# Performance work log

Measured on AMD Instinct MI355X. Metric: run time of the kernel, lower is better.

Reference implementation:

```python
import jax, jax.numpy as jnp
import numpy as np

N = 100000
E = 1600000
IN_DIM = 1024
H_DIM = 16
DIM2 = H_DIM * 8  # 128


def _xavier(key, shape):
    fan_in, fan_out = shape[-2], shape[-1]
    lim = (6.0 / (fan_in + fan_out)) ** 0.5
    return jax.random.uniform(key, shape, jnp.float32, -lim, lim)


def setup_inputs() -> dict:
    key = jax.random.key(0)
    ks = jax.random.split(key, 10)
    x = jax.random.normal(ks[0], (N, IN_DIM), jnp.float32)
    edge_index = jax.random.randint(ks[1], (2, E), 0, N)
    perm = jax.random.permutation(ks[2], N)
    W1 = _xavier(ks[3], (IN_DIM, DIM2)); b1 = jnp.zeros((DIM2,), jnp.float32)
    W2 = _xavier(ks[4], (DIM2, DIM2)); b2 = jnp.zeros((DIM2,), jnp.float32)
    W3 = _xavier(ks[5], (DIM2, H_DIM)); b3 = jnp.zeros((H_DIM,), jnp.float32)
    Wdo = _xavier(ks[6], (1, DIM2, DIM2)); bdo = jnp.zeros((1,), jnp.float32)
    Wdh = _xavier(ks[7], (1, H_DIM, H_DIM)); bdh = jnp.zeros((1,), jnp.float32)
    return dict(x=x, W1=W1, b1=b1, W2=W2, b2=b2, W3=W3, b3=b3,
                Wdo=Wdo, bdo=bdo, Wdh=Wdh, bdh=bdh,
                edge_index=edge_index, perm=perm)


def _graph_conv(x, W, b, src, dst, norm_src, norm_dst):
    # DGL GraphConv, norm='both': D_dst^{-1/2} A D_src^{-1/2} X W + b
    h = (x * norm_src[:, None]) @ W          # mult W first (in >= out)
    agg = jax.ops.segment_sum(h[src], dst, num_segments=N)
    return agg * norm_dst[:, None] + b


def _l2norm(x):
    n = jnp.sqrt(jnp.sum(x * x, axis=1, keepdims=True))
    return x / jnp.maximum(n, 1e-12)


def _bilinear(a, c, W, b):
    # nn.Bilinear(n_h, n_h, 1): out[n,k] = a[n] @ W[k] @ c[n] + b[k]
    return jnp.einsum('nd,kde,ne->nk', a, W, c) + b


def reference(x, W1, b1, W2, b2, W3, b3, Wdo, bdo, Wdh, bdh, edge_index, perm):
    src, dst = edge_index[0], edge_index[1]
    ones = jnp.ones((E,), jnp.float32)
    deg_out = jnp.maximum(jax.ops.segment_sum(ones, src, num_segments=N), 1.0)
    deg_in = jnp.maximum(jax.ops.segment_sum(ones, dst, num_segments=N), 1.0)
    ns, nd = deg_out ** -0.5, deg_in ** -0.5

    def encode(xin):
        o = _graph_conv(xin, W1, b1, src, dst, ns, nd)
        o = _graph_conv(o, W2, b2, src, dst, ns, nd) + o
        h = _graph_conv(o, W3, b3, src, dst, ns, nd)
        emb_o = jax.nn.relu(o)
        g_o = jax.nn.sigmoid(_l2norm(emb_o))
        emb_h = jax.nn.relu(h)
        g_h = jax.nn.sigmoid(_l2norm(emb_h))
        return h, emb_o, g_o, emb_h, g_h

    h, emb_o, g_o, emb_h, g_h = encode(x)
    h_a, emb_oa, g_oa, emb_ha, g_ha = encode(x[perm])

    def disc(c, h_pl, h_mi, W, b):
        return jnp.concatenate([_bilinear(h_pl, c, W, b), _bilinear(h_mi, c, W, b)], axis=1)

    ret_o = disc(g_o, emb_o, emb_oa, Wdo, bdo)
    ret_oa = disc(g_oa, emb_oa, emb_o, Wdo, bdo)
    ret_h = disc(g_h, emb_h, emb_ha, Wdh, bdh)
    ret_ha = disc(g_ha, emb_ha, emb_h, Wdh, bdh)
    return (h, ret_o, ret_h, ret_oa, ret_ha)
```

## Files before the change

kernel.cpp:

```cpp
#include <hip/hip_runtime.h>
#include <math.h>

#define NN 100000
#define EE 1600000
#define SCB 98
#define GB1 782
#define FB 3125

typedef __attribute__((ext_vector_type(8))) short bf16x8;
typedef __attribute__((ext_vector_type(4))) short bf16x4;
typedef __attribute__((ext_vector_type(4))) float f32x4;

__device__ __forceinline__ unsigned short f2bf(float x){
  union { float f; unsigned u; } v; v.f = x;
  unsigned r = v.u + 0x7FFFu + ((v.u >> 16) & 1u);
  return (unsigned short)(r >> 16);
}
__device__ __forceinline__ float bf2f(unsigned short h){
  union { unsigned u; float f; } v; v.u = ((unsigned)h) << 16; return v.f;
}
__device__ __forceinline__ float sigm(float x){ return 1.0f/(1.0f+__expf(-x)); }

__device__ __forceinline__ void barrier_lds_only(){
  asm volatile("s_waitcnt lgkmcnt(0)" ::: "memory");
  __builtin_amdgcn_s_barrier();
  __builtin_amdgcn_sched_barrier(0);
}

__global__ __launch_bounds__(256) void k_deg_wcvt(const int* __restrict__ src, const int* __restrict__ dst,
                      int* __restrict__ dout, int* __restrict__ din,
                      const float* __restrict__ W1, const float* __restrict__ W2,
                      const float* __restrict__ Wdo, const float* __restrict__ W3,
                      unsigned short* __restrict__ W1T, unsigned short* __restrict__ W2T,
                      unsigned short* __restrict__ WdoB, unsigned short* __restrict__ W3c){
  int b = blockIdx.x;
  if (b < EE/256){
    int e = b*256 + threadIdx.x;
    atomicAdd(&dout[src[e]],1); atomicAdd(&din[dst[e]],1);
  } else {
    int i = (b - EE/256)*256 + threadIdx.x;
    if (i < 131072){
      int c = i>>13, r = i&8191, col = r>>6, k = c*64 + (r&63);
      W1T[i] = f2bf(W1[(size_t)k*128 + col]);
    } else if (i < 147456){
      int j = i-131072;
      int c = j>>13, r = j&8191, col = r>>6, k = c*64 + (r&63);
      W2T[j] = f2bf(W2[(size_t)k*128 + col]);
    } else if (i < 163840){
      int j = i-147456;
      int c = j>>13, r = j&8191, col = r>>6, k = c*64 + (r&63);
      WdoB[j] = f2bf(Wdo[(size_t)col*128 + k]);
    } else if (i < 165888){
      int j = i-163840;
      int col = j>>7, k = j&127;
      W3c[j] = f2bf(W3[(size_t)k*16 + col]);
    }
  }
}

__global__ __launch_bounds__(1024) void k_scan1(const int* __restrict__ din, int* __restrict__ chunk,
                        int* __restrict__ bsum){
  __shared__ int wsum[16];
  int t = threadIdx.x, lane = t & 63, w = t >> 6;
  int i = blockIdx.x*1024 + t;
  int v = (i < NN) ? din[i] : 0;
  int x = v;
  #pragma unroll
  for (int off=1; off<64; off<<=1){
    int y = __shfl_up(x, off);
    if (lane>=off) x += y;
  }
  if (lane==63) wsum[w] = x;
  __syncthreads();
  int pre = 0;
  #pragma unroll
  for (int j=0;j<16;j++) if (j<w) pre += wsum[j];
  int incl = x + pre;
  if (i < NN) chunk[i] = incl;
  if (t == 1023) bsum[blockIdx.x] = incl;
}

__global__ __launch_bounds__(128) void k_scan2(const int* __restrict__ bsum, int* __restrict__ bpre,
                       int* __restrict__ row_ptr){
  __shared__ int w0tot;
  int t = threadIdx.x, lane = t & 63, w = t >> 6;
  int v = (t < SCB) ? bsum[t] : 0;
  int x = v;
  #pragma unroll
  for (int off=1; off<64; off<<=1){
    int y = __shfl_up(x, off);
    if (lane>=off) x += y;
  }
  if (w==0 && lane==63) w0tot = x;
  __syncthreads();
  int incl = x + (w ? w0tot : 0);
  if (t < SCB) bpre[t] = incl - v;
  if (t == 0) row_ptr[0] = 0;
}

__global__ __launch_bounds__(256) void k_scan3(const int* __restrict__ din, const int* __restrict__ chunk,
                       const int* __restrict__ bpre, const int* __restrict__ dout,
                       const int* __restrict__ perm,
                       int* __restrict__ row_ptr, int* __restrict__ cursor,
                       float* __restrict__ ns, float* __restrict__ nd, int* __restrict__ inv){
  int i = blockIdx.x*256 + threadIdx.x;
  if (i < NN){
    int d = din[i];
    int val = chunk[i] + bpre[i>>10];
    row_ptr[i+1] = val;
    cursor[i] = val - d;
    ns[i] = rsqrtf((float)max(dout[i],1));
    nd[i] = rsqrtf((float)max(d,1));
    inv[perm[i]] = i;
  }
}

__global__ __launch_bounds__(512,4) void k_g1fill(
    const float* __restrict__ A, const unsigned short* __restrict__ Wc,
    unsigned short* __restrict__ tz,
    const int* __restrict__ src, const int* __restrict__ dst,
    int* __restrict__ cursor, int* __restrict__ col)
{
  constexpr int NC = 16;
  __shared__ __align__(16) unsigned short As[2*128*72];
  __shared__ __align__(16) unsigned short Bs[2*128*64];
  if (blockIdx.x >= GB1){
    int e = (blockIdx.x - GB1)*512 + threadIdx.x;
    if (e < EE){
      int pos = atomicAdd(&cursor[dst[e]],1);
      col[pos] = src[e];
    }
    return;
  }
  int t = threadIdx.x, wave = t>>6, lane = t&63;
  int row0 = blockIdx.x*128;

  int srow = t>>4;
  int scol4 = (t&15)*4;
  int colB = t>>2;
  int s0B = (t&3)*2;

  f32x4 acc[8] = {};
  float4 S0[4], S1[4];
  bf16x8 w0{}, w1{};

#define ALOAD(SET, CC) { \
  _Pragma("unroll") \
  for (int p=0;p<4;p++){ \
    int rr = min(row0 + p*32 + srow, NN-1); \
    SET[p] = *(const float4*)(A + (size_t)rr*1024 + (CC)*64 + scol4); } }

#define AWRITE(SET, BUF) { \
  _Pragma("unroll") \
  for (int p=0;p<4;p++){ \
    short4 s4; \
    s4.x = (short)f2bf(SET[p].x); s4.y = (short)f2bf(SET[p].y); \
    s4.z = (short)f2bf(SET[p].z); s4.w = (short)f2bf(SET[p].w); \
    *(short4*)&As[(BUF)*9216 + (p*32+srow)*72 + scol4] = s4; } }

#define BLOAD(CC) { \
  const unsigned short* gp = Wc + (size_t)(CC)*8192 + (size_t)t*16; \
  w0 = *(const bf16x8*)(gp); \
  w1 = *(const bf16x8*)(gp+8); }

#define BWRITE(BUF) { \
  unsigned short* bb = &Bs[(BUF)*8192]; \
  *(bf16x8*)&bb[colB*64 + ((s0B     ^ (colB&7))<<3)] = w0; \
  *(bf16x8*)&bb[colB*64 + (((s0B+1) ^ (colB&7))<<3)] = w1; }

  ALOAD(S0, 0);
  BLOAD(0);
  AWRITE(S0, 0);
  BWRITE(0);
  ALOAD(S1, 1);
  BLOAD(1);
  barrier_lds_only();

  int slot0 = lane>>4;
  int c = lane & 15;
  int arow = wave*16 + (lane&15);
  #pragma unroll
  for (int cc=0; cc<NC; ++cc){
    if (cc+2 < NC){
      if (cc&1) { ALOAD(S1, cc+2); } else { ALOAD(S0, cc+2); }
    }
    int cur = cc&1;
    const unsigned short* ab = &As[cur*9216];
    const unsigned short* bb = &Bs[cur*8192];
    {
      bf16x8 af = *(const bf16x8*)&ab[arow*72 + (slot0<<3)];
      #pragma unroll
      for (int j=0;j<8;j++){
        int cj = j*16 + c;
        bf16x8 b = *(const bf16x8*)&bb[cj*64 + ((slot0 ^ (cj&7))<<3)];
        acc[j] = __builtin_amdgcn_mfma_f32_16x16x32_bf16(af, b, acc[j], 0, 0, 0);
      }
    }
    {
      bf16x8 af = *(const bf16x8*)&ab[arow*72 + 32 + (slot0<<3)];
      #pragma unroll
      for (int j=0;j<8;j++){
        int cj = j*16 + c;
        bf16x8 b = *(const bf16x8*)&bb[cj*64 + (((slot0+4) ^ (cj&7))<<3)];
        acc[j] = __builtin_amdgcn_mfma_f32_16x16x32_bf16(af, b, acc[j], 0, 0, 0);
      }
    }
    if (cc+1 < NC){
      int nb = (cc+1)&1;
      if (cc&1) { AWRITE(S0, nb); } else { AWRITE(S1, nb); }
      BWRITE(nb);
      barrier_lds_only();
      if (cc+2 < NC) BLOAD(cc+2);
    }
  }
#undef ALOAD
#undef AWRITE
#undef BLOAD
#undef BWRITE

  int rbase = row0 + wave*16 + (lane>>4)*4;
  #pragma unroll
  for (int j=0;j<8;j++){
    int colx = j*16 + c;
    #pragma unroll
    for (int r=0;r<4;r++){
      int row = rbase + r;
      if (row < NN) tz[(size_t)row*128 + colx] = f2bf(acc[j][r]);
    }
  }
}

__global__ __launch_bounds__(256) void k_agg1(
  const unsigned short* __restrict__ tz, const int* __restrict__ perm,
  const float* __restrict__ ns,
  const int* __restrict__ row_ptr, const int* __restrict__ col,
  const float* __restrict__ nd, const float* __restrict__ bias,
  unsigned short* __restrict__ ob)
{
  int wave = threadIdx.x>>6, lane = threadIdx.x&63;
  int row = blockIdx.x*4 + wave;
  if (row >= NN) return;
  int s = row_ptr[row], e = row_ptr[row+1];
  int es = lane>>5;
  int half = (lane>>4)&1;
  int c8 = (lane&15)*8;
  float acc[8] = {};
  bf16x8 zer = {};
  int i = s + es;

#define FETCH1(IDX, U, F) { \
  if ((IDX) < e){ \
    int sc = col[(IDX)]; \
    int rr = half ? perm[sc] : sc; \
    F = ns[sc]; \
    U = *(const bf16x8*)(tz + (size_t)rr*128 + c8); \
  } else { F = 0.0f; U = zer; } }

  bf16x8 u0, u1, u2, u3;
  float f0, f1, f2, f3;
  FETCH1(i,   u0, f0);
  FETCH1(i+2, u1, f1);
  FETCH1(i+4, u2, f2);
  FETCH1(i+6, u3, f3);
  while (i < e){
    bf16x8 w0, w1; float g0, g1;
    FETCH1(i+8,  w0, g0);
    FETCH1(i+10, w1, g1);
    #pragma unroll
    for (int j=0;j<8;j++)
      acc[j] += bf2f((unsigned short)u0[j])*f0 + bf2f((unsigned short)u1[j])*f1;
    u0=u2; f0=f2; u1=u3; f1=f3;
    u2=w0; f2=g0; u3=w1; f3=g1;
    i += 4;
  }
#undef FETCH1
  #pragma unroll
  for (int j=0;j<8;j++) acc[j] += __shfl_down(acc[j], 32);
  if (lane < 32){
    float ndr = nd[row];
    size_t oof = half ? (size_t)(NN+row)*128 + c8 : (size_t)row*128 + c8;
    bf16x8 wv;
    #pragma unroll
    for (int j=0;j<8;j++) wv[j] = (short)f2bf(acc[j]*ndr + bias[c8+j]);
    *(bf16x8*)(ob + oof) = wv;
  }
}

struct ARU { bf16x8 a; };
__device__ __forceinline__ void aload(ARU& r, const unsigned short* p){
  r.a = *(const bf16x8*)p;
}
template<int IM>
__device__ __forceinline__ bf16x8 aconv(const ARU& r, float rs){
  if constexpr (IM==0) return r.a;
  else {
    bf16x8 o;
    #pragma unroll
    for (int i=0;i<8;i++){
      float v = sigm(fmaxf(bf2f((unsigned short)r.a[i]),0.0f)*rs);
      o[i] = (short)f2bf(v);
    }
    return o;
  }
}
__device__ __forceinline__ bf16x8 araw(const ARU& r){ return r.a; }

template<int KDIM, int IN_MODE, int OUT_MODE>
__global__ __launch_bounds__(256,2) void k_gemmA(
    const unsigned short* __restrict__ A, const unsigned short* __restrict__ Wc,
    unsigned short* __restrict__ out0,
    const float* __restrict__ scale,
    const float* __restrict__ rn, int nrows,
    float* __restrict__ ro, float* __restrict__ roa,
    const unsigned short* __restrict__ W3c, const float* __restrict__ ns2,
    unsigned short* __restrict__ th)
{
  constexpr int NC = KDIM/64;
  __shared__ __align__(16) unsigned short Bs[2*128*64];
  __shared__ __align__(16) unsigned short W3s[OUT_MODE==3 ? 16*128 : 16];
  int t = threadIdx.x, wave = t>>6, lane = t&63;
  int row0 = blockIdx.x*64;
  int arow = row0 + wave*16 + (lane&15);
  int kof = (lane>>4)*8;
  int arow_c = min(arow, nrows-1);
  const unsigned short* ap = A + (size_t)arow_c*KDIM + kof;
  float rscale = 1.0f;
  if constexpr (IN_MODE==1) rscale = rn[arow_c];

  int scol = t>>3;
  int sw = ((t&7) ^ (scol&7))<<3;

  unsigned short* b0 = &Bs[0];
  unsigned short* b1 = &Bs[128*64];
  const unsigned short* bcur = b0; unsigned short* bnxt = b1;

  f32x4 acc[8] = {};
  f32x4 acc2 = {};
  ARU A0a{},A0b{},A1a{},A1b{},A2a{},A2b{};
  bf16x8 w0{},w1{},w2{},w3{};

  {
    const unsigned short* gp = Wc + (size_t)t*8;
    bf16x8 t0 = *(const bf16x8*)(gp);
    bf16x8 t1 = *(const bf16x8*)(gp+2048);
    bf16x8 t2 = *(const bf16x8*)(gp+4096);
    bf16x8 t3 = *(const bf16x8*)(gp+6144);
    *(bf16x8*)&b0[(0*32+scol)*64 + sw] = t0;
    *(bf16x8*)&b0[(1*32+scol)*64 + sw] = t1;
    *(bf16x8*)&b0[(2*32+scol)*64 + sw] = t2;
    *(bf16x8*)&b0[(3*32+scol)*64 + sw] = t3;
  }
  if constexpr (OUT_MODE==3){
    int wc = t>>4, wsl = t&15;
    bf16x8 v = *(const bf16x8*)(W3c + wc*128 + wsl*8);
    *(bf16x8*)&W3s[wc*128 + ((wsl ^ (wc&7))<<3)] = v;
  }
  aload(A0a, ap); aload(A0b, ap+32);
  if (NC>1){
    const unsigned short* gp = Wc + 8192 + (size_t)t*8;
    w0 = *(const bf16x8*)(gp);
    w1 = *(const bf16x8*)(gp+2048);
    w2 = *(const bf16x8*)(gp+4096);
    w3 = *(const bf16x8*)(gp+6144);
    aload(A1a, ap+64); aload(A1b, ap+96);
  }
  __syncthreads();

  int slot0 = lane>>4;
  int c = lane & 15;
  #pragma unroll
  for (int cc=0; cc<NC; ++cc){
    if (cc+2 < NC){
      aload(A2a, ap + (cc+2)*64);
      aload(A2b, ap + (cc+2)*64 + 32);
    }
    {
      bf16x8 af = aconv<IN_MODE>(A0a, rscale);
      #pragma unroll
      for (int j=0;j<8;j++){
        int cj = j*16 + c;
        bf16x8 b = *(const bf16x8*)&bcur[cj*64 + ((slot0 ^ (cj&7))<<3)];
        acc[j] = __builtin_amdgcn_mfma_f32_16x16x32_bf16(af, b, acc[j], 0, 0, 0);
      }
      if constexpr (OUT_MODE==3){
        int sl = cc*8 + slot0;
        bf16x8 b = *(const bf16x8*)&W3s[c*128 + ((sl ^ (c&7))<<3)];
        acc2 = __builtin_amdgcn_mfma_f32_16x16x32_bf16(araw(A0a), b, acc2, 0, 0, 0);
      }
    }
    {
      bf16x8 af = aconv<IN_MODE>(A0b, rscale);
      #pragma unroll
      for (int j=0;j<8;j++){
        int cj = j*16 + c;
        bf16x8 b = *(const bf16x8*)&bcur[cj*64 + (((slot0+4) ^ (cj&7))<<3)];
        acc[j] = __builtin_amdgcn_mfma_f32_16x16x32_bf16(af, b, acc[j], 0, 0, 0);
      }
      if constexpr (OUT_MODE==3){
        int sl = cc*8 + 4 + slot0;
        bf16x8 b = *(const bf16x8*)&W3s[c*128 + ((sl ^ (c&7))<<3)];
        acc2 = __builtin_amdgcn_mfma_f32_16x16x32_bf16(araw(A0b), b, acc2, 0, 0, 0);
      }
    }
    if (cc+1 < NC){
      *(bf16x8*)&bnxt[(0*32+scol)*64 + sw] = w0;
      *(bf16x8*)&bnxt[(1*32+scol)*64 + sw] = w1;
      *(bf16x8*)&bnxt[(2*32+scol)*64 + sw] = w2;
      *(bf16x8*)&bnxt[(3*32+scol)*64 + sw] = w3;
      barrier_lds_only();
      const unsigned short* tmp = bcur; bcur = bnxt; bnxt = (unsigned short*)tmp;
      if (cc+2 < NC){
        const unsigned short* gp = Wc + (size_t)(cc+2)*8192 + (size_t)t*8;
        w0 = *(const bf16x8*)(gp);
        w1 = *(const bf16x8*)(gp+2048);
        w2 = *(const bf16x8*)(gp+4096);
        w3 = *(const bf16x8*)(gp+6144);
      }
    }
    A0a=A1a; A0b=A1b; A1a=A2a; A1b=A2b;
  }

  if constexpr (OUT_MODE==3){
    #pragma unroll
    for (int r=0;r<4;r++){
      int row = row0 + wave*16 + (lane>>4)*4 + r;
      int sidx = row>=NN ? row-NN : row;
      float v = acc2[r]*ns2[sidx];
      size_t tof = row<NN ? (size_t)row*32 + c : (size_t)(row-NN)*32 + 16 + c;
      th[tof] = f2bf(v);
    }
    __syncthreads();
    unsigned short* Os = &Bs[0];
    unsigned short* Oo = &Bs[8192];
    for (int p=t; p<2048; p+=256){
      int r = (p>>4)&63, seg = p&15;
      int row = row0 + r;
      int srcrow = (p<1024) ? row : (row<NN ? row+NN : row-NN);
      unsigned short* dst = (p<1024) ? Os : Oo;
      *(bf16x8*)&dst[r*128 + ((seg ^ (r&7))<<3)] = *(const bf16x8*)&A[(size_t)srcrow*128 + seg*8];
    }
    __syncthreads();
    float bb = scale[0];
    #pragma unroll
    for (int r=0;r<4;r++){
      int lr = wave*16 + (lane>>4)*4 + r;
      float dsame=0.f, doth=0.f;
      #pragma unroll
      for (int j=0;j<8;j++){
        float v = acc[j][r];
        int colj = j*16 + c;
        int idx = lr*128 + (((colj>>3) ^ (lr&7))<<3) + (colj&7);
        dsame += fmaxf(bf2f(Os[idx]),0.f)*v;
        doth  += fmaxf(bf2f(Oo[idx]),0.f)*v;
      }
      #pragma unroll
      for (int off=1; off<16; off<<=1){
        dsame += __shfl_xor(dsame, off);
        doth  += __shfl_xor(doth, off);
      }
      if (c==0){
        int row = row0 + lr;
        if (row < NN){
          ro[(size_t)row*2+0] = dsame + bb;
          ro[(size_t)row*2+1] = doth + bb;
        } else {
          int m = row - NN;
          roa[(size_t)m*2+0] = dsame + bb;
          roa[(size_t)m*2+1] = doth + bb;
        }
      }
    }
  } else {
    int rbase = row0 + wave*16 + (lane>>4)*4;
    #pragma unroll
    for (int j=0;j<8;j++){
      int colx = j*16 + c;
      #pragma unroll
      for (int r=0;r<4;r++){
        int row = rbase + r;
        if (row < nrows){
          float v = acc[j][r];
          int sidx = row >= NN ? row - NN : row;
          size_t zof = row < NN ? (size_t)row*256 + colx : (size_t)(row-NN)*256 + 128 + colx;
          out0[zof] = f2bf(v * scale[sidx]);
        }
      }
    }
  }
}

__global__ __launch_bounds__(256) void k_agg128(
  const unsigned short* __restrict__ z,
  const int* __restrict__ row_ptr, const int* __restrict__ col,
  const float* __restrict__ nd, const float* __restrict__ bias,
  unsigned short* __restrict__ ob, float* __restrict__ rn)
{
  int wave = threadIdx.x>>6, lane = threadIdx.x&63;
  int row = blockIdx.x*4 + wave;
  if (row >= NN) return;
  int s = row_ptr[row], e = row_ptr[row+1];
  int es = lane>>5;
  int half = (lane>>4)&1;
  int c8 = (lane&15)*8;
  size_t lof = (size_t)half*128 + c8;
  float acc[8] = {};
  int i = s + es;
  int c0 = (i   < e) ? col[i]   : -1;
  int c1 = (i+2 < e) ? col[i+2] : -1;
  int c2 = (i+4 < e) ? col[i+4] : -1;
  int c3 = (i+6 < e) ? col[i+6] : -1;
  bf16x8 u0 = {}, u1 = {}, u2 = {}, u3 = {};
  if (c0 >= 0) u0 = *(const bf16x8*)(z + (size_t)c0*256 + lof);
  if (c1 >= 0) u1 = *(const bf16x8*)(z + (size_t)c1*256 + lof);
  if (c2 >= 0) u2 = *(const bf16x8*)(z + (size_t)c2*256 + lof);
  if (c3 >= 0) u3 = *(const bf16x8*)(z + (size_t)c3*256 + lof);
  while (c0 >= 0){
    int n0 = (i+8  < e) ? col[i+8]  : -1;
    int n1 = (i+10 < e) ? col[i+10] : -1;
    bf16x8 w0 = {}, w1 = {};
    if (n0 >= 0) w0 = *(const bf16x8*)(z + (size_t)n0*256 + lof);
    if (n1 >= 0) w1 = *(const bf16x8*)(z + (size_t)n1*256 + lof);
    #pragma unroll
    for (int j=0;j<8;j++) acc[j] += bf2f((unsigned short)u0[j]) + bf2f((unsigned short)u1[j]);
    c0 = c2; c1 = c3; u0 = u2; u1 = u3;
    c2 = n0; c3 = n1; u2 = w0; u3 = w1;
    i += 4;
  }
  #pragma unroll
  for (int j=0;j<8;j++) acc[j] += __shfl_down(acc[j], 32);
  if (lane < 32){
    float ndr = nd[row];
    size_t oof = half ? (size_t)(NN+row)*128 + c8 : (size_t)row*128 + c8;
    float ra[8];
    #pragma unroll
    for (int j=0;j<8;j++) ra[j] = acc[j]*ndr + bias[c8+j];
    {
      bf16x8 pv = *(const bf16x8*)(ob + oof);
      #pragma unroll
      for (int j=0;j<8;j++) ra[j] += bf2f((unsigned short)pv[j]);
    }
    bf16x8 wv;
    #pragma unroll
    for (int j=0;j<8;j++) wv[j] = (short)f2bf(ra[j]);
    *(bf16x8*)(ob + oof) = wv;
    {
      float sa = 0.f;
      #pragma unroll
      for (int j=0;j<8;j++){ float x1 = fmaxf(ra[j],0.f); sa += x1*x1; }
      sa += __shfl_down(sa, 8);
      sa += __shfl_down(sa, 4);
      sa += __shfl_down(sa, 2);
      sa += __shfl_down(sa, 1);
      if ((lane&15)==0) rn[half ? NN+row : row] = 1.0f/fmaxf(sqrtf(sa),1e-12f);
    }
  }
}

__global__ __launch_bounds__(256) void k_agg16(
  const unsigned short* __restrict__ th,
  const int* __restrict__ row_ptr, const int* __restrict__ col,
  const float* __restrict__ nd, const float* __restrict__ b3,
  const float* __restrict__ Wdh, const float* __restrict__ bdh,
  float* __restrict__ hout, float* __restrict__ rh, float* __restrict__ rha)
{
  __shared__ float Ws[256];
  __shared__ float hbuf[4][32];
  __shared__ float gbuf[4][32];
  int t = threadIdx.x;
  Ws[t] = Wdh[t];
  __syncthreads();
  int wave = t>>6, lane = t&63;
  int row = blockIdx.x*4 + wave;
  if (row >= NN) return;
  int s = row_ptr[row], e = row_ptr[row+1];
  int es = lane>>3, l8 = lane&7;
  float a4[4] = {};
  int i = s + es;
  int c0 = (i   <e)? col[i]    : -1;
  int c1 = (i+8 <e)? col[i+8]  : -1;
  int c2 = (i+16<e)? col[i+16] : -1;
  int c3 = (i+24<e)? col[i+24] : -1;
  bf16x4 u0 = {}, u1 = {}, u2 = {}, u3 = {};
  if (c0 >= 0) u0 = *(const bf16x4*)(th + (size_t)c0*32 + l8*4);
  if (c1 >= 0) u1 = *(const bf16x4*)(th + (size_t)c1*32 + l8*4);
  if (c2 >= 0) u2 = *(const bf16x4*)(th + (size_t)c2*32 + l8*4);
  if (c3 >= 0) u3 = *(const bf16x4*)(th + (size_t)c3*32 + l8*4);
  while (c0 >= 0){
    int n0 = (i+32<e)? col[i+32] : -1;
    int n1 = (i+40<e)? col[i+40] : -1;
    bf16x4 w0 = {}, w1 = {};
    if (n0 >= 0) w0 = *(const bf16x4*)(th + (size_t)n0*32 + l8*4);
    if (n1 >= 0) w1 = *(const bf16x4*)(th + (size_t)n1*32 + l8*4);
    #pragma unroll
    for (int j=0;j<4;j++) a4[j] += bf2f((unsigned short)u0[j]) + bf2f((unsigned short)u1[j]);
    c0 = c2; c1 = c3; u0 = u2; u1 = u3;
    c2 = n0; c3 = n1; u2 = w0; u3 = w1;
    i += 16;
  }
  #pragma unroll
  for (int j=0;j<4;j++){
    a4[j] += __shfl_down(a4[j], 32);
    a4[j] += __shfl_down(a4[j], 16);
    a4[j] += __shfl_down(a4[j], 8);
  }
  if (lane < 8){
    float ndr = nd[row];
    int half = l8>>2, c0x = (l8&3)*4;
    float4 r;
    r.x = a4[0]*ndr + b3[c0x+0];
    r.y = a4[1]*ndr + b3[c0x+1];
    r.z = a4[2]*ndr + b3[c0x+2];
    r.w = a4[3]*ndr + b3[c0x+3];
    if (half==0) *(float4*)&hout[(size_t)row*16 + c0x] = r;
    int hb = half*16 + c0x;
    hbuf[wave][hb+0]=r.x; hbuf[wave][hb+1]=r.y; hbuf[wave][hb+2]=r.z; hbuf[wave][hb+3]=r.w;
  }
  if (lane < 16){
    int d = lane;
    float e1v = fmaxf(hbuf[wave][d],    0.f);
    float e2v = fmaxf(hbuf[wave][16+d], 0.f);
    float s1 = e1v*e1v, s2 = e2v*e2v;
    #pragma unroll
    for (int off=1; off<16; off<<=1){
      s1 += __shfl_xor(s1, off);
      s2 += __shfl_xor(s2, off);
    }
    float r1 = 1.0f/fmaxf(sqrtf(s1),1e-12f);
    float r2 = 1.0f/fmaxf(sqrtf(s2),1e-12f);
    gbuf[wave][d]    = sigm(e1v*r1);
    gbuf[wave][16+d] = sigm(e2v*r2);
    float vh1=0.f, vh2=0.f;
    #pragma unroll
    for (int e2i=0;e2i<16;e2i++){
      float w = Ws[d*16+e2i];
      vh1 += w*gbuf[wave][e2i];
      vh2 += w*gbuf[wave][16+e2i];
    }
    float q00 = e1v*vh1, q01 = e2v*vh1, q10 = e2v*vh2, q11 = e1v*vh2;
    #pragma unroll
    for (int off=1; off<16; off<<=1){
      q00 += __shfl_xor(q00, off);
      q01 += __shfl_xor(q01, off);
      q10 += __shfl_xor(q10, off);
      q11 += __shfl_xor(q11, off);
    }
    if (lane==0){
      float bb = bdh[0];
      rh [(size_t)row*2+0]=q00+bb; rh [(size_t)row*2+1]=q01+bb;
      rha[(size_t)row*2+0]=q10+bb; rha[(size_t)row*2+1]=q11+bb;
    }
  }
}

extern "C" void kernel_launch(void* const* d_in, const int* in_sizes, int n_in,
                              void* d_out, int out_size, void* d_ws, size_t ws_size,
                              hipStream_t stream){
  const float* x   = (const float*)d_in[0];
  const float* W1  = (const float*)d_in[1];
  const float* b1  = (const float*)d_in[2];
  const float* W2  = (const float*)d_in[3];
  const float* b2  = (const float*)d_in[4];
  const float* W3  = (const float*)d_in[5];
  const float* b3  = (const float*)d_in[6];
  const float* Wdo = (const float*)d_in[7];
  const float* bdo = (const float*)d_in[8];
  const float* Wdh = (const float*)d_in[9];
  const float* bdh = (const float*)d_in[10];
  const int* ei    = (const int*)d_in[11];
  const int* perm  = (const int*)d_in[12];
  const int* esrc = ei;
  const int* edst = ei + EE;

  char* ws = (char*)d_ws;
  size_t off = 0;
  auto alloc = [&](size_t bytes)->void*{ void* p = ws + off; off += (bytes + 255) & ~(size_t)255; return p; };
  unsigned short* z  = (unsigned short*)alloc((size_t)NN*256*2);
  unsigned short* ob = (unsigned short*)alloc((size_t)2*NN*128*2);
  unsigned short* tz = (unsigned short*)alloc((size_t)NN*128*2);
  unsigned short* th = (unsigned short*)alloc((size_t)NN*32*2);
  int* deg = (int*)alloc((size_t)2*NN*4);
  int* dout_ = deg; int* din_ = deg + NN;
  float* ns = (float*)alloc((size_t)NN*4);
  float* nd = (float*)alloc((size_t)NN*4);
  int* inv  = (int*)alloc((size_t)NN*4);
  float* rn = (float*)alloc((size_t)2*NN*4);
  int* cursor = (int*)alloc((size_t)NN*4);
  int* row_ptr = (int*)alloc((size_t)(NN+1)*4);
  int* colx = (int*)alloc((size_t)EE*4);
  int* chunk = (int*)alloc((size_t)NN*4);
  int* bsum = (int*)alloc((size_t)SCB*4);
  int* bpre = (int*)alloc((size_t)SCB*4);
  unsigned short* W1T = (unsigned short*)alloc((size_t)1024*128*2);
  unsigned short* W2T = (unsigned short*)alloc((size_t)128*128*2);
  unsigned short* WdoB = (unsigned short*)alloc((size_t)128*128*2);
  unsigned short* W3c = (unsigned short*)alloc((size_t)16*128*2);

  float* out_h   = (float*)d_out;
  float* out_ro  = out_h  + (size_t)NN*16;
  float* out_rh  = out_ro + (size_t)NN*2;
  float* out_roa = out_rh + (size_t)NN*2;
  float* out_rha = out_roa+ (size_t)NN*2;

  hipMemsetAsync(deg, 0, (size_t)2*NN*4, stream);
  k_deg_wcvt<<<EE/256 + 648, 256, 0, stream>>>(esrc, edst, dout_, din_,
                                               W1, W2, Wdo, W3, W1T, W2T, WdoB, W3c);
  k_scan1<<<SCB, 1024, 0, stream>>>(din_, chunk, bsum);
  k_scan2<<<1, 128, 0, stream>>>(bsum, bpre, row_ptr);
  k_scan3<<<(NN+255)/256, 256, 0, stream>>>(din_, chunk, bpre, dout_, perm, row_ptr, cursor, ns, nd, inv);

  int gb2 = (2*NN)/64;
  k_g1fill<<<GB1 + FB, 512, 0, stream>>>(x, W1T, tz, esrc, edst, cursor, colx);
  k_agg1<<<(NN+3)/4,256,0,stream>>>(tz, perm, ns, row_ptr, colx, nd, b1, ob);
  k_gemmA<128,0,1><<<gb2,256,0,stream>>>(ob, W2T, z, ns, nullptr, 2*NN,
                                         nullptr, nullptr, nullptr, nullptr, nullptr);
  k_agg128<<<(NN+3)/4,256,0,stream>>>(z, row_ptr, colx, nd, b2, ob, rn);
  k_gemmA<128,1,3><<<gb2,256,0,stream>>>(ob, WdoB, nullptr, bdo, rn, 2*NN,
                                         out_ro, out_roa, W3c, ns, th);
  k_agg16<<<(NN+3)/4,256,0,stream>>>(th, row_ptr, colx, nd, b3, Wdh, bdh, out_h, out_rh, out_rha);
}
```

Baseline: 699.1 us.

## Split first GEMM by output-column halves with direct A register loads

Measured after the change: 751.5 us. 7.5% more time.

```diff
diff --git a/kernel.cpp b/kernel.cpp
--- a/kernel.cpp
+++ b/kernel.cpp
@@ -4,7 +4,7 @@
 #define NN 100000
 #define EE 1600000
 #define SCB 98
-#define GB1 782
+#define GB1 1564
 #define FB 3125
 
 typedef __attribute__((ext_vector_type(8))) short bf16x8;
@@ -40,8 +40,12 @@
   } else {
     int i = (b - EE/256)*256 + threadIdx.x;
     if (i < 131072){
-      int c = i>>13, r = i&8191, col = r>>6, k = c*64 + (r&63);
-      W1T[i] = f2bf(W1[(size_t)k*128 + col]);
+      int kh = i>>16, r = i&65535;
+      int chh = r>>15, r2 = r&32767;
+      int colh = r2>>9, s = (r2>>3)&63, e2 = i&7;
+      int kslot = s ^ (colh&7);
+      int k = kh*512 + kslot*8 + e2;
+      W1T[i] = f2bf(W1[(size_t)k*128 + chh*64 + colh]);
     } else if (i < 147456){
       int j = i-131072;
       int c = j>>13, r = j&8191, col = r>>6, k = c*64 + (r&63);
@@ -115,15 +119,13 @@
   }
 }
 
-__global__ __launch_bounds__(512,4) void k_g1fill(
+__global__ __launch_bounds__(512,2) void k_g1fill(
     const float* __restrict__ A, const unsigned short* __restrict__ Wc,
     unsigned short* __restrict__ tz,
     const int* __restrict__ src, const int* __restrict__ dst,
     int* __restrict__ cursor, int* __restrict__ col)
 {
-  constexpr int NC = 16;
-  __shared__ __align__(16) unsigned short As[2*128*72];
-  __shared__ __align__(16) unsigned short Bs[2*128*64];
+  __shared__ __align__(16) unsigned short Bs[64*512];
   if (blockIdx.x >= GB1){
     int e = (blockIdx.x - GB1)*512 + threadIdx.x;
     if (e < EE){
@@ -133,95 +135,78 @@
     return;
   }
   int t = threadIdx.x, wave = t>>6, lane = t&63;
-  int row0 = blockIdx.x*128;
-
-  int srow = t>>4;
-  int scol4 = (t&15)*4;
-  int colB = t>>2;
-  int s0B = (t&3)*2;
-
-  f32x4 acc[8] = {};
-  float4 S0[4], S1[4];
-  bf16x8 w0{}, w1{};
-
-#define ALOAD(SET, CC) { \
-  _Pragma("unroll") \
-  for (int p=0;p<4;p++){ \
-    int rr = min(row0 + p*32 + srow, NN-1); \
-    SET[p] = *(const float4*)(A + (size_t)rr*1024 + (CC)*64 + scol4); } }
-
-#define AWRITE(SET, BUF) { \
-  _Pragma("unroll") \
-  for (int p=0;p<4;p++){ \
-    short4 s4; \
-    s4.x = (short)f2bf(SET[p].x); s4.y = (short)f2bf(SET[p].y); \
-    s4.z = (short)f2bf(SET[p].z); s4.w = (short)f2bf(SET[p].w); \
-    *(short4*)&As[(BUF)*9216 + (p*32+srow)*72 + scol4] = s4; } }
-
-#define BLOAD(CC) { \
-  const unsigned short* gp = Wc + (size_t)(CC)*8192 + (size_t)t*16; \
-  w0 = *(const bf16x8*)(gp); \
-  w1 = *(const bf16x8*)(gp+8); }
-
-#define BWRITE(BUF) { \
-  unsigned short* bb = &Bs[(BUF)*8192]; \
-  *(bf16x8*)&bb[colB*64 + ((s0B     ^ (colB&7))<<3)] = w0; \
-  *(bf16x8*)&bb[colB*64 + (((s0B+1) ^ (colB&7))<<3)] = w1; }
-
-  ALOAD(S0, 0);
-  BLOAD(0);
-  AWRITE(S0, 0);
-  BWRITE(0);
-  ALOAD(S1, 1);
-  BLOAD(1);
+  int rows0 = (blockIdx.x>>1)*128;
+  int ch = blockIdx.x & 1;
+
+  int arow = min(rows0 + wave*16 + (lane&15), NN-1);
+  int kof = (lane>>4)*8;
+  const float* ap = A + (size_t)arow*1024 + kof;
+  int c = lane & 15;
+  int slot0 = lane>>4;
+
+  f32x4 acc[4] = {};
+  float4 P0[4], P1[4];
+
+#define LD(P, CC) { \
+  P[0] = *(const float4*)(ap + (CC)*64); \
+  P[1] = *(const float4*)(ap + (CC)*64 + 4); \
+  P[2] = *(const float4*)(ap + (CC)*64 + 32); \
+  P[3] = *(const float4*)(ap + (CC)*64 + 36); }
+
+#define CHUNK(CC, P) { \
+  bf16x8 af0, af1; \
+  { float v0[8] = {P[0].x,P[0].y,P[0].z,P[0].w,P[1].x,P[1].y,P[1].z,P[1].w}; \
+    float v1[8] = {P[2].x,P[2].y,P[2].z,P[2].w,P[3].x,P[3].y,P[3].z,P[3].w}; \
+    _Pragma("unroll") \
+    for (int q=0;q<8;q++){ af0[q] = (short)f2bf(v0[q]); af1[q] = (short)f2bf(v1[q]); } } \
+  if ((CC)+2 < 16) LD(P, (CC)+2); \
+  { int kb = ((CC)&7)*8; \
+    _Pragma("unroll") \
+    for (int j=0;j<4;j++){ \
+      int cj = j*16 + c; \
+      int s0 = (kb + slot0) ^ (cj&7); \
+      bf16x8 b = *(const bf16x8*)&Bs[cj*512 + (s0<<3)]; \
+      acc[j] = __builtin_amdgcn_mfma_f32_16x16x32_bf16(af0, b, acc[j], 0, 0, 0); \
+    } \
+    _Pragma("unroll") \
+    for (int j=0;j<4;j++){ \
+      int cj = j*16 + c; \
+      int s1 = (kb + 4 + slot0) ^ (cj&7); \
+      bf16x8 b = *(const bf16x8*)&Bs[cj*512 + (s1<<3)]; \
+      acc[j] = __builtin_amdgcn_mfma_f32_16x16x32_bf16(af1, b, acc[j], 0, 0, 0); \
+    } } }
+
+  {
+    const unsigned short* wsrc = Wc + (size_t)ch*32768;
+    #pragma unroll
+    for (int p=0;p<8;p++)
+      *(bf16x8*)&Bs[p*4096 + t*8] = *(const bf16x8*)&wsrc[p*4096 + t*8];
+  }
+  LD(P0, 0); LD(P1, 1);
+  __syncthreads();
+
+  CHUNK(0,P0)  CHUNK(1,P1)  CHUNK(2,P0)  CHUNK(3,P1)
+  CHUNK(4,P0)  CHUNK(5,P1)  CHUNK(6,P0)  CHUNK(7,P1)
+
+  __syncthreads();
+  {
+    const unsigned short* wsrc = Wc + 65536 + (size_t)ch*32768;
+    #pragma unroll
+    for (int p=0;p<8;p++)
+      *(bf16x8*)&Bs[p*4096 + t*8] = *(const bf16x8*)&wsrc[p*4096 + t*8];
+  }
   barrier_lds_only();
 
-  int slot0 = lane>>4;
-  int c = lane & 15;
-  int arow = wave*16 + (lane&15);
+  CHUNK(8,P0)  CHUNK(9,P1)  CHUNK(10,P0) CHUNK(11,P1)
+  CHUNK(12,P0) CHUNK(13,P1) CHUNK(14,P0) CHUNK(15,P1)
+
+#undef LD
+#undef CHUNK
+
+  int rbase = rows0 + wave*16 + (lane>>4)*4;
   #pragma unroll
-  for (int cc=0; cc<NC; ++cc){
-    if (cc+2 < NC){
-      if (cc&1) { ALOAD(S1, cc+2); } else { ALOAD(S0, cc+2); }
-    }
-    int cur = cc&1;
-    const unsigned short* ab = &As[cur*9216];
-    const unsigned short* bb = &Bs[cur*8192];
-    {
-      bf16x8 af = *(const bf16x8*)&ab[arow*72 + (slot0<<3)];
-      #pragma unroll
-      for (int j=0;j<8;j++){
-        int cj = j*16 + c;
-        bf16x8 b = *(const bf16x8*)&bb[cj*64 + ((slot0 ^ (cj&7))<<3)];
-        acc[j] = __builtin_amdgcn_mfma_f32_16x16x32_bf16(af, b, acc[j], 0, 0, 0);
-      }
-    }
-    {
-      bf16x8 af = *(const bf16x8*)&ab[arow*72 + 32 + (slot0<<3)];
-      #pragma unroll
-      for (int j=0;j<8;j++){
-        int cj = j*16 + c;
-        bf16x8 b = *(const bf16x8*)&bb[cj*64 + (((slot0+4) ^ (cj&7))<<3)];
-        acc[j] = __builtin_amdgcn_mfma_f32_16x16x32_bf16(af, b, acc[j], 0, 0, 0);
-      }
-    }
-    if (cc+1 < NC){
-      int nb = (cc+1)&1;
-      if (cc&1) { AWRITE(S0, nb); } else { AWRITE(S1, nb); }
-      BWRITE(nb);
-      barrier_lds_only();
-      if (cc+2 < NC) BLOAD(cc+2);
-    }
-  }
-#undef ALOAD
-#undef AWRITE
-#undef BLOAD
-#undef BWRITE
-
-  int rbase = row0 + wave*16 + (lane>>4)*4;
-  #pragma unroll
-  for (int j=0;j<8;j++){
-    int colx = j*16 + c;
+  for (int j=0;j<4;j++){
+    int colx = ch*64 + j*16 + c;
     #pragma unroll
     for (int r=0;r<4;r++){
       int row = rbase + r;
```

## Split first GEMM across degree-count and CSR-fill kernels; store perm in edge list

Applied to the files above, without the earlier changes.

After: 649.9 us. 7.0% less time.

```diff
diff --git a/kernel.cpp b/kernel.cpp
--- a/kernel.cpp
+++ b/kernel.cpp
@@ -4,7 +4,7 @@
 #define NN 100000
 #define EE 1600000
 #define SCB 98
-#define GB1 782
+#define NG1 391
 #define FB 3125
 
 typedef __attribute__((ext_vector_type(8))) short bf16x8;
@@ -27,34 +27,27 @@
   __builtin_amdgcn_sched_barrier(0);
 }
 
-__global__ __launch_bounds__(256) void k_deg_wcvt(const int* __restrict__ src, const int* __restrict__ dst,
-                      int* __restrict__ dout, int* __restrict__ din,
+__global__ __launch_bounds__(256) void k_wcvt(
                       const float* __restrict__ W1, const float* __restrict__ W2,
                       const float* __restrict__ Wdo, const float* __restrict__ W3,
                       unsigned short* __restrict__ W1T, unsigned short* __restrict__ W2T,
                       unsigned short* __restrict__ WdoB, unsigned short* __restrict__ W3c){
-  int b = blockIdx.x;
-  if (b < EE/256){
-    int e = b*256 + threadIdx.x;
-    atomicAdd(&dout[src[e]],1); atomicAdd(&din[dst[e]],1);
-  } else {
-    int i = (b - EE/256)*256 + threadIdx.x;
-    if (i < 131072){
-      int c = i>>13, r = i&8191, col = r>>6, k = c*64 + (r&63);
-      W1T[i] = f2bf(W1[(size_t)k*128 + col]);
-    } else if (i < 147456){
-      int j = i-131072;
-      int c = j>>13, r = j&8191, col = r>>6, k = c*64 + (r&63);
-      W2T[j] = f2bf(W2[(size_t)k*128 + col]);
-    } else if (i < 163840){
-      int j = i-147456;
-      int c = j>>13, r = j&8191, col = r>>6, k = c*64 + (r&63);
-      WdoB[j] = f2bf(Wdo[(size_t)col*128 + k]);
-    } else if (i < 165888){
-      int j = i-163840;
-      int col = j>>7, k = j&127;
-      W3c[j] = f2bf(W3[(size_t)k*16 + col]);
-    }
+  int i = blockIdx.x*256 + threadIdx.x;
+  if (i < 131072){
+    int c = i>>13, r = i&8191, col = r>>6, k = c*64 + (r&63);
+    W1T[i] = f2bf(W1[(size_t)k*128 + col]);
+  } else if (i < 147456){
+    int j = i-131072;
+    int c = j>>13, r = j&8191, col = r>>6, k = c*64 + (r&63);
+    W2T[j] = f2bf(W2[(size_t)k*128 + col]);
+  } else if (i < 163840){
+    int j = i-147456;
+    int c = j>>13, r = j&8191, col = r>>6, k = c*64 + (r&63);
+    WdoB[j] = f2bf(Wdo[(size_t)col*128 + k]);
+  } else if (i < 165888){
+    int j = i-163840;
+    int col = j>>7, k = j&127;
+    W3c[j] = f2bf(W3[(size_t)k*16 + col]);
   }
 }
 
@@ -115,25 +108,33 @@
   }
 }
 
-__global__ __launch_bounds__(512,4) void k_g1fill(
+template<int TAIL>
+__global__ __launch_bounds__(512,4) void k_g1(
     const float* __restrict__ A, const unsigned short* __restrict__ Wc,
     unsigned short* __restrict__ tz,
     const int* __restrict__ src, const int* __restrict__ dst,
-    int* __restrict__ cursor, int* __restrict__ col)
+    int* __restrict__ p0, int* __restrict__ p1,
+    int2* __restrict__ colx2, const int* __restrict__ perm, int rowBase)
 {
   constexpr int NC = 16;
   __shared__ __align__(16) unsigned short As[2*128*72];
   __shared__ __align__(16) unsigned short Bs[2*128*64];
-  if (blockIdx.x >= GB1){
-    int e = (blockIdx.x - GB1)*512 + threadIdx.x;
+  if (blockIdx.x >= NG1){
+    int e = (blockIdx.x - NG1)*512 + threadIdx.x;
     if (e < EE){
-      int pos = atomicAdd(&cursor[dst[e]],1);
-      col[pos] = src[e];
+      if constexpr (TAIL==0){
+        atomicAdd(&p0[src[e]],1);
+        atomicAdd(&p1[dst[e]],1);
+      } else {
+        int s = src[e];
+        int pos = atomicAdd(&p0[dst[e]],1);
+        colx2[pos] = make_int2(s, perm[s]);
+      }
     }
     return;
   }
   int t = threadIdx.x, wave = t>>6, lane = t&63;
-  int row0 = blockIdx.x*128;
+  int row0 = (rowBase + blockIdx.x)*128;
 
   int srow = t>>4;
   int scol4 = (t&15)*4;
@@ -231,9 +232,9 @@
 }
 
 __global__ __launch_bounds__(256) void k_agg1(
-  const unsigned short* __restrict__ tz, const int* __restrict__ perm,
+  const unsigned short* __restrict__ tz,
   const float* __restrict__ ns,
-  const int* __restrict__ row_ptr, const int* __restrict__ col,
+  const int* __restrict__ row_ptr, const int2* __restrict__ colx2,
   const float* __restrict__ nd, const float* __restrict__ bias,
   unsigned short* __restrict__ ob)
 {
@@ -250,9 +251,9 @@
 
 #define FETCH1(IDX, U, F) { \
   if ((IDX) < e){ \
-    int sc = col[(IDX)]; \
-    int rr = half ? perm[sc] : sc; \
-    F = ns[sc]; \
+    int2 cc = colx2[(IDX)]; \
+    int rr = half ? cc.y : cc.x; \
+    F = ns[cc.x]; \
     U = *(const bf16x8*)(tz + (size_t)rr*128 + c8); \
   } else { F = 0.0f; U = zer; } }
 
@@ -491,7 +492,7 @@
 
 __global__ __launch_bounds__(256) void k_agg128(
   const unsigned short* __restrict__ z,
-  const int* __restrict__ row_ptr, const int* __restrict__ col,
+  const int* __restrict__ row_ptr, const int2* __restrict__ colx2,
   const float* __restrict__ nd, const float* __restrict__ bias,
   unsigned short* __restrict__ ob, float* __restrict__ rn)
 {
@@ -505,18 +506,18 @@
   size_t lof = (size_t)half*128 + c8;
   float acc[8] = {};
   int i = s + es;
-  int c0 = (i   < e) ? col[i]   : -1;
-  int c1 = (i+2 < e) ? col[i+2] : -1;
-  int c2 = (i+4 < e) ? col[i+4] : -1;
-  int c3 = (i+6 < e) ? col[i+6] : -1;
+  int c0 = (i   < e) ? colx2[i].x   : -1;
+  int c1 = (i+2 < e) ? colx2[i+2].x : -1;
+  int c2 = (i+4 < e) ? colx2[i+4].x : -1;
+  int c3 = (i+6 < e) ? colx2[i+6].x : -1;
   bf16x8 u0 = {}, u1 = {}, u2 = {}, u3 = {};
   if (c0 >= 0) u0 = *(const bf16x8*)(z + (size_t)c0*256 + lof);
   if (c1 >= 0) u1 = *(const bf16x8*)(z + (size_t)c1*256 + lof);
   if (c2 >= 0) u2 = *(const bf16x8*)(z + (size_t)c2*256 + lof);
   if (c3 >= 0) u3 = *(const bf16x8*)(z + (size_t)c3*256 + lof);
   while (c0 >= 0){
-    int n0 = (i+8  < e) ? col[i+8]  : -1;
-    int n1 = (i+10 < e) ? col[i+10] : -1;
+    int n0 = (i+8  < e) ? colx2[i+8].x  : -1;
+    int n1 = (i+10 < e) ? colx2[i+10].x : -1;
     bf16x8 w0 = {}, w1 = {};
     if (n0 >= 0) w0 = *(const bf16x8*)(z + (size_t)n0*256 + lof);
     if (n1 >= 0) w1 = *(const bf16x8*)(z + (size_t)n1*256 + lof);
@@ -558,7 +559,7 @@
 
 __global__ __launch_bounds__(256) void k_agg16(
   const unsigned short* __restrict__ th,
-  const int* __restrict__ row_ptr, const int* __restrict__ col,
+  const int* __restrict__ row_ptr, const int2* __restrict__ colx2,
   const float* __restrict__ nd, const float* __restrict__ b3,
   const float* __restrict__ Wdh, const float* __restrict__ bdh,
   float* __restrict__ hout, float* __restrict__ rh, float* __restrict__ rha)
@@ -576,18 +577,18 @@
   int es = lane>>3, l8 = lane&7;
   float a4[4] = {};
   int i = s + es;
-  int c0 = (i   <e)? col[i]    : -1;
-  int c1 = (i+8 <e)? col[i+8]  : -1;
-  int c2 = (i+16<e)? col[i+16] : -1;
-  int c3 = (i+24<e)? col[i+24] : -1;
+  int c0 = (i   <e)? colx2[i].x    : -1;
+  int c1 = (i+8 <e)? colx2[i+8].x  : -1;
+  int c2 = (i+16<e)? colx2[i+16].x : -1;
+  int c3 = (i+24<e)? colx2[i+24].x : -1;
   bf16x4 u0 = {}, u1 = {}, u2 = {}, u3 = {};
   if (c0 >= 0) u0 = *(const bf16x4*)(th + (size_t)c0*32 + l8*4);
   if (c1 >= 0) u1 = *(const bf16x4*)(th + (size_t)c1*32 + l8*4);
   if (c2 >= 0) u2 = *(const bf16x4*)(th + (size_t)c2*32 + l8*4);
   if (c3 >= 0) u3 = *(const bf16x4*)(th + (size_t)c3*32 + l8*4);
   while (c0 >= 0){
-    int n0 = (i+32<e)? col[i+32] : -1;
-    int n1 = (i+40<e)? col[i+40] : -1;
+    int n0 = (i+32<e)? colx2[i+32].x : -1;
+    int n1 = (i+40<e)? colx2[i+40].x : -1;
     bf16x4 w0 = {}, w1 = {};
     if (n0 >= 0) w0 = *(const bf16x4*)(th + (size_t)n0*32 + l8*4);
     if (n1 >= 0) w1 = *(const bf16x4*)(th + (size_t)n1*32 + l8*4);
@@ -686,7 +687,7 @@
   float* rn = (float*)alloc((size_t)2*NN*4);
   int* cursor = (int*)alloc((size_t)NN*4);
   int* row_ptr = (int*)alloc((size_t)(NN+1)*4);
-  int* colx = (int*)alloc((size_t)EE*4);
+  int2* colx2 = (int2*)alloc((size_t)EE*8);
   int* chunk = (int*)alloc((size_t)NN*4);
   int* bsum = (int*)alloc((size_t)SCB*4);
   int* bpre = (int*)alloc((size_t)SCB*4);
@@ -702,19 +703,21 @@
   float* out_rha = out_roa+ (size_t)NN*2;
 
   hipMemsetAsync(deg, 0, (size_t)2*NN*4, stream);
-  k_deg_wcvt<<<EE/256 + 648, 256, 0, stream>>>(esrc, edst, dout_, din_,
-                                               W1, W2, Wdo, W3, W1T, W2T, WdoB, W3c);
+  k_wcvt<<<648, 256, 0, stream>>>(W1, W2, Wdo, W3, W1T, W2T, WdoB, W3c);
+  k_g1<0><<<NG1 + FB, 512, 0, stream>>>(x, W1T, tz, esrc, edst, dout_, din_,
+                                        nullptr, perm, 0);
   k_scan1<<<SCB, 1024, 0, stream>>>(din_, chunk, bsum);
   k_scan2<<<1, 128, 0, stream>>>(bsum, bpre, row_ptr);
   k_scan3<<<(NN+255)/256, 256, 0, stream>>>(din_, chunk, bpre, dout_, perm, row_ptr, cursor, ns, nd, inv);
+  k_g1<1><<<NG1 + FB, 512, 0, stream>>>(x, W1T, tz, esrc, edst, cursor, nullptr,
+                                        colx2, perm, NG1);
 
   int gb2 = (2*NN)/64;
-  k_g1fill<<<GB1 + FB, 512, 0, stream>>>(x, W1T, tz, esrc, edst, cursor, colx);
-  k_agg1<<<(NN+3)/4,256,0,stream>>>(tz, perm, ns, row_ptr, colx, nd, b1, ob);
+  k_agg1<<<(NN+3)/4,256,0,stream>>>(tz, ns, row_ptr, colx2, nd, b1, ob);
   k_gemmA<128,0,1><<<gb2,256,0,stream>>>(ob, W2T, z, ns, nullptr, 2*NN,
                                          nullptr, nullptr, nullptr, nullptr, nullptr);
-  k_agg128<<<(NN+3)/4,256,0,stream>>>(z, row_ptr, colx, nd, b2, ob, rn);
+  k_agg128<<<(NN+3)/4,256,0,stream>>>(z, row_ptr, colx2, nd, b2, ob, rn);
   k_gemmA<128,1,3><<<gb2,256,0,stream>>>(ob, WdoB, nullptr, bdo, rn, 2*NN,
                                          out_ro, out_roa, W3c, ns, th);
-  k_agg16<<<(NN+3)/4,256,0,stream>>>(th, row_ptr, colx, nd, b3, Wdh, bdh, out_h, out_rh, out_rha);
-}
+  k_agg16<<<(NN+3)/4,256,0,stream>>>(th, row_ptr, colx2, nd, b3, Wdh, bdh, out_h, out_rh, out_rha);
+}
```
